# Optimization experiments

Hardware: AMD Instinct MI355X
Metric: run time of the kernel (lower is better)

## Reference

```python
import jax, jax.numpy as jnp
from jax import lax
import numpy as np

K_F = 3                      # propagation kernel
NUM = K_F * K_F - 1          # 8 non-reference neighbors
IDX_REF = NUM // 2           # 4
PROP_TIME = 18
GAMMA = 0.5                  # affinity_gamma (TGASS)
EPS_AFF = 1e-8


def setup_inputs() -> dict:
    key = jax.random.key(0)
    k1, k2, k3, k4, k5 = jax.random.split(key, 5)
    B, H, W = 4, 352, 1216
    feat_init = jax.random.uniform(k1, (B, 1, H, W), jnp.float32) * 10.0   # initial depth
    guidance = jax.random.normal(k2, (B, NUM, H, W), jnp.float32)
    confidence = jax.random.uniform(k3, (B, 1, H, W), jnp.float32)
    # conv_offset_aff: Conv2d(ch_g=8 -> 3*num=24, k=3, pad=1). Zero-init in the
    # module is a training init; use small random weights for a meaningful test.
    w_oa = jax.random.normal(k4, (3 * NUM, NUM, 3, 3), jnp.float32) * 0.05
    b_oa = jax.random.normal(k5, (3 * NUM,), jnp.float32) * 0.01
    aff_scale = jnp.array([GAMMA * NUM], jnp.float32)  # TGASS learnable scale
    return {"feat_init": feat_init, "guidance": guidance, "confidence": confidence,
            "w_oa": w_oa, "b_oa": b_oa, "aff_scale": aff_scale}


def _offset_affinity(guidance, w_oa, b_oa, aff_scale):
    B, _, H, W = guidance.shape
    oa = lax.conv_general_dilated(guidance, w_oa, (1, 1), "SAME",
                                  dimension_numbers=("NCHW", "OIHW", "NCHW"))
    oa = oa + b_oa[None, :, None, None]
    o1, o2, aff = jnp.split(oa, 3, axis=1)            # each [B, 8, H, W]
    offset = jnp.concatenate([o1, o2], axis=1).reshape(B, NUM, 2, H, W)
    zeros_ref = jnp.zeros((B, 1, 2, H, W), offset.dtype)
    offset = jnp.concatenate([offset[:, :IDX_REF], zeros_ref, offset[:, IDX_REF:]],
                             axis=1).reshape(B, -1, H, W)  # [B, 2*9, H, W]
    # TGASS affinity
    aff = jnp.tanh(aff) / (aff_scale[0] + EPS_AFF)
    aff_abs_sum = jnp.sum(jnp.abs(aff), axis=1, keepdims=True) + 1e-4
    aff_abs_sum = jnp.maximum(aff_abs_sum, 1.0)       # TGASS clamp to >= 1
    aff = aff / aff_abs_sum
    aff_ref = 1.0 - jnp.sum(aff, axis=1, keepdims=True)
    aff = jnp.concatenate([aff[:, :IDX_REF], aff_ref, aff[:, IDX_REF:]], axis=1)
    return offset, aff                                 # [B,18,H,W], [B,9,H,W]


def _bilinear(f, ys, xs):
    # f: [H, W]; ys, xs: [K, H, W] float sample coords. Zero outside bounds (DCNv2).
    H, W = f.shape
    y0 = jnp.floor(ys); x0 = jnp.floor(xs)
    wy1 = ys - y0; wy0 = 1.0 - wy1
    wx1 = xs - x0; wx0 = 1.0 - wx1

    def g(yi, xi):
        valid = (yi >= 0) & (yi <= H - 1) & (xi >= 0) & (xi <= W - 1)
        yc = jnp.clip(yi, 0, H - 1).astype(jnp.int32)
        xc = jnp.clip(xi, 0, W - 1).astype(jnp.int32)
        return jnp.where(valid, f[yc, xc], 0.0)

    return (wy0 * wx0 * g(y0, x0) + wy0 * wx1 * g(y0, x0 + 1)
            + wy1 * wx0 * g(y0 + 1, x0) + wy1 * wx1 * g(y0 + 1, x0 + 1))


def _dcn(feat, offset, aff):
    # Modulated deformable conv with w=ones, b=0, stride=1, pad=1, groups=1.
    # feat [B,1,H,W], offset [B,2*9,H,W] ((dy,dx) pairs), aff [B,9,H,W] modulation.
    B, _, H, W = feat.shape
    KK = K_F * K_F
    off = offset.reshape(B, KK, 2, H, W)
    k = jnp.arange(KK)
    ky = (k // K_F - 1).astype(feat.dtype)            # kernel taps, pad=1
    kx = (k % K_F - 1).astype(feat.dtype)
    yg, xg = jnp.meshgrid(jnp.arange(H, dtype=feat.dtype),
                          jnp.arange(W, dtype=feat.dtype), indexing="ij")
    ys = yg[None, None] + ky[None, :, None, None] + off[:, :, 0]  # [B,9,H,W]
    xs = xg[None, None] + kx[None, :, None, None] + off[:, :, 1]
    sampled = jax.vmap(_bilinear)(feat[:, 0], ys, xs)             # [B,9,H,W]
    return jnp.sum(aff * sampled, axis=1, keepdims=True)          # [B,1,H,W]


def reference(feat_init, guidance, confidence, w_oa, b_oa, aff_scale):
    offset, aff = _offset_affinity(guidance, w_oa, b_oa, aff_scale)

    def step(feat, _):
        feat = _dcn(feat * confidence, offset, aff)
        return feat, None

    feat, _ = lax.scan(step, feat_init, None, length=PROP_TIME)
    return feat
```

## Files before the change

### kernel.cpp

```cpp
#include <hip/hip_runtime.h>

#define BB 4
#define HH 352
#define WW 1216
#define HW (HH * WW)
#define NPIX (BB * HW)
#define TX 4

#define PAD_T 5
#define PAD_L 8
#define HP (HH + 2 * PAD_T)
#define WP (WW + 2 * PAD_L)
#define HWP (HP * WP)

#define TROWS 17
#define TCOLS 76
#define TSIZE (TROWS * TCOLS)


__global__ __launch_bounds__(256) void conv_fused_kernel(
    const float* __restrict__ guid, const float* __restrict__ w,
    const float* __restrict__ bias, const float* __restrict__ scale_p,
    unsigned* __restrict__ tab)
{
    int tid = threadIdx.x;
    int bid = blockIdx.x;
    int xcd = bid & 7;
    int u = bid >> 3;
    int role = u & 1;
    int blk = xcd * 209 + (u >> 1);
    int gg = blk * 256 + tid;
    int row = gg / 304;
    int x0 = (gg % 304) * TX;
    int y = row % HH;
    int b = row / HH;
    const float* gb = guid + (size_t)b * 8 * HW;

    if (role == 0) {
        float acc[16][TX];
#pragma unroll
        for (int o = 0; o < 16; ++o) {
            float bv = bias[o];
#pragma unroll
            for (int tx = 0; tx < TX; ++tx) acc[o][tx] = bv;
        }

#pragma unroll 1
        for (int c = 0; c < 8; ++c) {
            float g[3][6];
#pragma unroll
            for (int r = 0; r < 3; ++r) {
                int yy = y + r - 1;
                bool rv = (yy >= 0) && (yy < HH);
                const float* gr = gb + (size_t)c * HW + (size_t)yy * WW;
                if (rv) {
                    const float4 m = *(const float4*)(gr + x0);
                    g[r][1] = m.x; g[r][2] = m.y; g[r][3] = m.z; g[r][4] = m.w;
                    g[r][0] = (x0 > 0) ? gr[x0 - 1] : 0.f;
                    g[r][5] = (x0 + TX < WW) ? gr[x0 + TX] : 0.f;
                } else {
#pragma unroll
                    for (int i = 0; i < 6; ++i) g[r][i] = 0.f;
                }
            }
#pragma unroll
            for (int r = 0; r < 3; ++r) {
#pragma unroll
                for (int i = 0; i < 3; ++i) {
                    int tap = r * 3 + i;
#pragma unroll
                    for (int o = 0; o < 16; ++o) {
                        float wv = w[o * 72 + c * 9 + tap];
#pragma unroll
                        for (int tx = 0; tx < TX; ++tx)
                            acc[o][tx] = fmaf(wv, g[r][i + tx], acc[o][tx]);
                    }
                }
            }
        }

        int idx0 = row * WW + x0;
#pragma unroll
        for (int tx = 0; tx < TX; ++tx) {
            unsigned cw8[8];
#pragma unroll
            for (int n = 0; n < 8; ++n) {
                int k = (n < 4) ? n : n + 1;
                float ky = (float)(k / 3 - 1), kx = (float)(k % 3 - 1);
                float yr = ky + acc[2 * n][tx];
                float xr = kx + acc[2 * n + 1][tx];
                int yq = (int)lrintf((yr + 4.f) * 8192.f);
                int xq = (int)lrintf((xr + 4.f) * 8192.f);
                yq = min(max(yq, 0), 65535);
                xq = min(max(xq, 0), 65535);
                cw8[n] = (unsigned)yq | ((unsigned)xq << 16);
            }
            unsigned* tp = tab + (size_t)(idx0 + tx) * 12;
            *(uint4*)(tp)     = make_uint4(cw8[0], cw8[1], cw8[2], cw8[3]);
            *(uint4*)(tp + 4) = make_uint4(cw8[4], cw8[5], cw8[6], cw8[7]);
        }
    } else {
        float acc[8][TX];
#pragma unroll
        for (int o = 0; o < 8; ++o) {
            float bv = bias[16 + o];
#pragma unroll
            for (int tx = 0; tx < TX; ++tx) acc[o][tx] = bv;
        }

#pragma unroll 1
        for (int c = 0; c < 8; ++c) {
            float g[3][6];
#pragma unroll
            for (int r = 0; r < 3; ++r) {
                int yy = y + r - 1;
                bool rv = (yy >= 0) && (yy < HH);
                const float* gr = gb + (size_t)c * HW + (size_t)yy * WW;
                if (rv) {
                    const float4 m = *(const float4*)(gr + x0);
                    g[r][1] = m.x; g[r][2] = m.y; g[r][3] = m.z; g[r][4] = m.w;
                    g[r][0] = (x0 > 0) ? gr[x0 - 1] : 0.f;
                    g[r][5] = (x0 + TX < WW) ? gr[x0 + TX] : 0.f;
                } else {
#pragma unroll
                    for (int i = 0; i < 6; ++i) g[r][i] = 0.f;
                }
            }
#pragma unroll
            for (int r = 0; r < 3; ++r) {
#pragma unroll
                for (int i = 0; i < 3; ++i) {
                    int tap = r * 3 + i;
#pragma unroll
                    for (int o = 0; o < 8; ++o) {
                        float wv = w[(16 + o) * 72 + c * 9 + tap];
#pragma unroll
                        for (int tx = 0; tx < TX; ++tx)
                            acc[o][tx] = fmaf(wv, g[r][i + tx], acc[o][tx]);
                    }
                }
            }
        }

        float sc = scale_p[0] + 1e-8f;
        int idx0 = row * WW + x0;
#pragma unroll
        for (int tx = 0; tx < TX; ++tx) {
            float a[8];
            float asum = 1e-4f;
#pragma unroll
            for (int n = 0; n < 8; ++n) {
                a[n] = tanhf(acc[n][tx]) / sc;
                asum += fabsf(a[n]);
            }
            asum = fmaxf(asum, 1.0f);
            unsigned q8[8];
#pragma unroll
            for (int n = 0; n < 8; ++n) {
                a[n] = a[n] / asum;
                int q = (int)lrintf((a[n] + 1.f) * 20000.f);
                q = min(max(q, 0), 65535);
                q8[n] = (unsigned)q;
            }
            unsigned* tp = tab + (size_t)(idx0 + tx) * 12 + 8;
            *(uint4*)(tp) = make_uint4(q8[0] | (q8[1] << 16), q8[2] | (q8[3] << 16),
                                       q8[4] | (q8[5] << 16), q8[6] | (q8[7] << 16));
        }
    }
}

template <bool MULCONF>
__global__ __launch_bounds__(512) void prop_step_kernel(
    const float* __restrict__ fsrc, const unsigned* __restrict__ tab,
    const float* __restrict__ conf, float* __restrict__ dst)
{
    __shared__ float tile[TSIZE];

    int bid = blockIdx.x;
    int xcd = bid & 7;
    int s = bid >> 3;
    int gid = xcd * 418 + s;
    int b = gid / 836;
    int r2 = gid % 836;
    int yband = r2 / 19;
    int xb = r2 % 19;
    int t = threadIdx.x;
    int lx = t & 63, ly = t >> 6;
    int x = xb * 64 + lx;
    int y = yband * 8 + ly;
    int idx = (b * HH + y) * WW + x;

    const unsigned* tp = tab + (size_t)idx * 12;
    uint4 t0 = *(const uint4*)(tp);
    uint4 t1 = *(const uint4*)(tp + 4);
    uint4 t2 = *(const uint4*)(tp + 8);
    float cv = MULCONF ? conf[idx] : 0.f;

    {
        const float* gsrc = fsrc + (size_t)b * HWP
                          + (size_t)(yband * 8 + 1) * WP + (xb * 64 + 4);
        for (int i = t; i < TSIZE; i += 512)
            tile[i] = gsrc[(i / TCOLS) * WP + (i % TCOLS)];
    }

    unsigned cw[8] = {t0.x, t0.y, t0.z, t0.w, t1.x, t1.y, t1.z, t1.w};
    float ak[9];
    ak[0] = fmaf((float)(t2.x & 0xffffu), 5e-5f, -1.f);
    ak[1] = fmaf((float)(t2.x >> 16),     5e-5f, -1.f);
    ak[2] = fmaf((float)(t2.y & 0xffffu), 5e-5f, -1.f);
    ak[3] = fmaf((float)(t2.y >> 16),     5e-5f, -1.f);
    ak[5] = fmaf((float)(t2.z & 0xffffu), 5e-5f, -1.f);
    ak[6] = fmaf((float)(t2.z >> 16),     5e-5f, -1.f);
    ak[7] = fmaf((float)(t2.w & 0xffffu), 5e-5f, -1.f);
    ak[8] = fmaf((float)(t2.w >> 16),     5e-5f, -1.f);
    ak[4] = 1.f - (((ak[0] + ak[1]) + (ak[2] + ak[3]))
                 + ((ak[5] + ak[6]) + (ak[7] + ak[8])));

    __syncthreads();

    float fy = (float)ly;
    float fx = (float)lx;
    float res = ak[4] * tile[(ly + 4) * TCOLS + (lx + 4)];
#pragma unroll
    for (int n = 0; n < 8; ++n) {
        float ys = fmaf((float)(cw[n] & 0xffffu), 1.f / 8192.f, fy);
        float xs = fmaf((float)(cw[n] >> 16),     1.f / 8192.f, fx);
        float y0f = floorf(ys), x0f = floorf(xs);
        float wy1 = ys - y0f, wx1 = xs - x0f;
        float wy0 = 1.f - wy1, wx0 = 1.f - wx1;
        int o = (int)y0f * TCOLS + (int)x0f;
        float v00 = tile[o],         v01 = tile[o + 1];
        float v10 = tile[o + TCOLS], v11 = tile[o + TCOLS + 1];
        float sv = wy0 * (wx0 * v00 + wx1 * v01) + wy1 * (wx0 * v10 + wx1 * v11);
        int k = (n < 4) ? n : n + 1;
        res = fmaf(ak[k], sv, res);
    }
    if (MULCONF) {
        res *= cv;
        dst[(size_t)b * HWP + (y + PAD_T) * WP + (x + PAD_L)] = res;
    } else {
        dst[idx] = res;
    }
}

__global__ __launch_bounds__(256) void zero_kernel(float4* __restrict__ p, int n4)
{
    int i = blockIdx.x * blockDim.x + threadIdx.x;
    if (i < n4) p[i] = make_float4(0.f, 0.f, 0.f, 0.f);
}

__global__ __launch_bounds__(256) void mulpad_kernel(
    const float* __restrict__ a, const float* __restrict__ c, float* __restrict__ o)
{
    int t = threadIdx.x;
    int x = blockIdx.x * 64 + (t & 63);
    int y = blockIdx.y * 4 + (t >> 6);
    int b = blockIdx.z;
    int idx = (b * HH + y) * WW + x;
    o[(size_t)b * HWP + (y + PAD_T) * WP + (x + PAD_L)] = a[idx] * c[idx];
}

extern "C" void kernel_launch(void* const* d_in, const int* in_sizes, int n_in,
                              void* d_out, int out_size, void* d_ws, size_t ws_size,
                              hipStream_t stream)
{
    const float* feat_init  = (const float*)d_in[0];
    const float* guidance   = (const float*)d_in[1];
    const float* confidence = (const float*)d_in[2];
    const float* w_oa       = (const float*)d_in[3];
    const float* b_oa       = (const float*)d_in[4];
    const float* aff_scale  = (const float*)d_in[5];
    float* out = (float*)d_out;

    const size_t N = (size_t)NPIX;
    unsigned* tab = (unsigned*)d_ws;
    float* fc0 = (float*)(tab + 12 * N);
    float* fc1 = fc0 + (size_t)BB * HWP;

    const dim3 mgrid(WW / 64, HH / 4, BB);
    const int n4 = 2 * BB * HWP / 4;
    zero_kernel<<<(n4 + 255) / 256, 256, 0, stream>>>((float4*)fc0, n4);
    mulpad_kernel<<<mgrid, 256, 0, stream>>>(feat_init, confidence, fc0);
    conv_fused_kernel<<<2 * 1672, 256, 0, stream>>>(
        guidance, w_oa, b_oa, aff_scale, tab);

    const int pblocks = (WW / 64) * (HH / 8) * BB;
    float* bufs[2] = {fc0, fc1};
    const int T = 18;
    for (int i = 0; i < T; ++i) {
        const float* src = bufs[i & 1];
        if (i < T - 1) {
            float* dst = bufs[(i + 1) & 1];
            prop_step_kernel<true><<<pblocks, 512, 0, stream>>>(
                src, tab, confidence, dst);
        } else {
            prop_step_kernel<false><<<pblocks, 512, 0, stream>>>(
                src, tab, confidence, out);
        }
    }
}
```

Before: 533.7 us.

## Process four tiles per block with double-buffered LDS prefetch; fuse init kernels

```diff
diff --git a/kernel.cpp b/kernel.cpp
--- a/kernel.cpp
+++ b/kernel.cpp
@@ -16,6 +16,7 @@
 #define TROWS 17
 #define TCOLS 76
 #define TSIZE (TROWS * TCOLS)
+#define NTILES 3344
 
 
 __global__ __launch_bounds__(256) void conv_fused_kernel(
@@ -169,58 +170,68 @@
     }
 }
 
+struct TileLoad {
+    uint4 c0, c1, c2;
+    float cf;
+    float r0, r1, r2;
+    int idx;
+    long long poff;
+};
+
 template <bool MULCONF>
-__global__ __launch_bounds__(512) void prop_step_kernel(
+__device__ __forceinline__ TileLoad tile_issue(
+    int gid, int lx, int ly, int t,
     const float* __restrict__ fsrc, const unsigned* __restrict__ tab,
-    const float* __restrict__ conf, float* __restrict__ dst)
-{
-    __shared__ float tile[TSIZE];
-
-    int bid = blockIdx.x;
-    int xcd = bid & 7;
-    int s = bid >> 3;
-    int gid = xcd * 418 + s;
-    int b = gid / 836;
-    int r2 = gid % 836;
-    int yband = r2 / 19;
-    int xb = r2 % 19;
-    int t = threadIdx.x;
-    int lx = t & 63, ly = t >> 6;
-    int x = xb * 64 + lx;
-    int y = yband * 8 + ly;
-    int idx = (b * HH + y) * WW + x;
-
-    const unsigned* tp = tab + (size_t)idx * 12;
-    uint4 t0 = *(const uint4*)(tp);
-    uint4 t1 = *(const uint4*)(tp + 4);
-    uint4 t2 = *(const uint4*)(tp + 8);
-    float cv = MULCONF ? conf[idx] : 0.f;
-
-    {
-        const float* gsrc = fsrc + (size_t)b * HWP
-                          + (size_t)(yband * 8 + 1) * WP + (xb * 64 + 4);
-        for (int i = t; i < TSIZE; i += 512)
-            tile[i] = gsrc[(i / TCOLS) * WP + (i % TCOLS)];
-    }
-
-    unsigned cw[8] = {t0.x, t0.y, t0.z, t0.w, t1.x, t1.y, t1.z, t1.w};
+    const float* __restrict__ conf)
+{
+    TileLoad T;
+    int b = gid / 836, r2 = gid % 836;
+    int yb = r2 / 19, xb = r2 % 19;
+    int x = xb * 64 + lx, y = yb * 8 + ly;
+    T.idx = (b * HH + y) * WW + x;
+    T.poff = (long long)b * HWP + (long long)(y + PAD_T) * WP + (x + PAD_L);
+    const unsigned* tp = tab + (size_t)T.idx * 12;
+    T.c0 = *(const uint4*)(tp);
+    T.c1 = *(const uint4*)(tp + 4);
+    T.c2 = *(const uint4*)(tp + 8);
+    T.cf = MULCONF ? conf[T.idx] : 0.f;
+    const float* gs = fsrc + (size_t)b * HWP
+                    + (size_t)(yb * 8 + 1) * WP + (xb * 64 + 4);
+    T.r0 = gs[(t / TCOLS) * WP + (t % TCOLS)];
+    T.r1 = gs[((t + 512) / TCOLS) * WP + ((t + 512) % TCOLS)];
+    T.r2 = (t + 1024 < TSIZE)
+         ? gs[((t + 1024) / TCOLS) * WP + ((t + 1024) % TCOLS)] : 0.f;
+    return T;
+}
+
+__device__ __forceinline__ void tile_write(float* __restrict__ buf,
+                                           const TileLoad& T, int t)
+{
+    buf[t] = T.r0;
+    buf[t + 512] = T.r1;
+    if (t + 1024 < TSIZE) buf[t + 1024] = T.r2;
+}
+
+template <bool MULCONF>
+__device__ __forceinline__ void tile_compute(
+    const float* __restrict__ buf, const TileLoad& T,
+    float fy, float fx, int ly, int lx, float* __restrict__ dst)
+{
+    unsigned cw[8] = {T.c0.x, T.c0.y, T.c0.z, T.c0.w,
+                      T.c1.x, T.c1.y, T.c1.z, T.c1.w};
     float ak[9];
-    ak[0] = fmaf((float)(t2.x & 0xffffu), 5e-5f, -1.f);
-    ak[1] = fmaf((float)(t2.x >> 16),     5e-5f, -1.f);
-    ak[2] = fmaf((float)(t2.y & 0xffffu), 5e-5f, -1.f);
-    ak[3] = fmaf((float)(t2.y >> 16),     5e-5f, -1.f);
-    ak[5] = fmaf((float)(t2.z & 0xffffu), 5e-5f, -1.f);
-    ak[6] = fmaf((float)(t2.z >> 16),     5e-5f, -1.f);
-    ak[7] = fmaf((float)(t2.w & 0xffffu), 5e-5f, -1.f);
-    ak[8] = fmaf((float)(t2.w >> 16),     5e-5f, -1.f);
+    ak[0] = fmaf((float)(T.c2.x & 0xffffu), 5e-5f, -1.f);
+    ak[1] = fmaf((float)(T.c2.x >> 16),     5e-5f, -1.f);
+    ak[2] = fmaf((float)(T.c2.y & 0xffffu), 5e-5f, -1.f);
+    ak[3] = fmaf((float)(T.c2.y >> 16),     5e-5f, -1.f);
+    ak[5] = fmaf((float)(T.c2.z & 0xffffu), 5e-5f, -1.f);
+    ak[6] = fmaf((float)(T.c2.z >> 16),     5e-5f, -1.f);
+    ak[7] = fmaf((float)(T.c2.w & 0xffffu), 5e-5f, -1.f);
+    ak[8] = fmaf((float)(T.c2.w >> 16),     5e-5f, -1.f);
     ak[4] = 1.f - (((ak[0] + ak[1]) + (ak[2] + ak[3]))
                  + ((ak[5] + ak[6]) + (ak[7] + ak[8])));
 
-    __syncthreads();
-
-    float fy = (float)ly;
-    float fx = (float)lx;
-    float res = ak[4] * tile[(ly + 4) * TCOLS + (lx + 4)];
+    float res = ak[4] * buf[(ly + 4) * TCOLS + (lx + 4)];
 #pragma unroll
     for (int n = 0; n < 8; ++n) {
         float ys = fmaf((float)(cw[n] & 0xffffu), 1.f / 8192.f, fy);
@@ -229,35 +240,93 @@
         float wy1 = ys - y0f, wx1 = xs - x0f;
         float wy0 = 1.f - wy1, wx0 = 1.f - wx1;
         int o = (int)y0f * TCOLS + (int)x0f;
-        float v00 = tile[o],         v01 = tile[o + 1];
-        float v10 = tile[o + TCOLS], v11 = tile[o + TCOLS + 1];
-        float sv = wy0 * (wx0 * v00 + wx1 * v01) + wy1 * (wx0 * v10 + wx1 * v11);
+        float v00 = buf[o],         v01 = buf[o + 1];
+        float v10 = buf[o + TCOLS], v11 = buf[o + TCOLS + 1];
+        float sv = wy0 * (wx0 * v00 + wx1 * v01)
+                 + wy1 * (wx0 * v10 + wx1 * v11);
         int k = (n < 4) ? n : n + 1;
         res = fmaf(ak[k], sv, res);
     }
-    if (MULCONF) {
-        res *= cv;
-        dst[(size_t)b * HWP + (y + PAD_T) * WP + (x + PAD_L)] = res;
-    } else {
-        dst[idx] = res;
-    }
-}
-
-__global__ __launch_bounds__(256) void zero_kernel(float4* __restrict__ p, int n4)
-{
-    int i = blockIdx.x * blockDim.x + threadIdx.x;
-    if (i < n4) p[i] = make_float4(0.f, 0.f, 0.f, 0.f);
-}
-
-__global__ __launch_bounds__(256) void mulpad_kernel(
-    const float* __restrict__ a, const float* __restrict__ c, float* __restrict__ o)
-{
+    if (MULCONF)
+        dst[T.poff] = res * T.cf;
+    else
+        dst[T.idx] = res;
+}
+
+#define LDSBAR() do { \
+    asm volatile("s_waitcnt lgkmcnt(0)" ::: "memory"); \
+    __builtin_amdgcn_s_barrier(); \
+    __builtin_amdgcn_sched_barrier(0); \
+} while (0)
+
+template <bool MULCONF>
+__global__ __launch_bounds__(512) void prop_step_kernel(
+    const float* __restrict__ fsrc, const unsigned* __restrict__ tab,
+    const float* __restrict__ conf, float* __restrict__ dst)
+{
+    __shared__ float buf0[TSIZE];
+    __shared__ float buf1[TSIZE];
+
+    int bid = blockIdx.x;
+    int xcd = bid & 7;
+    int s = bid >> 3;
+    int base = xcd * 418 + 4 * s;
+    bool hasC = (4 * s + 2) < 418;
+    bool hasD = (4 * s + 3) < 418;
     int t = threadIdx.x;
-    int x = blockIdx.x * 64 + (t & 63);
-    int y = blockIdx.y * 4 + (t >> 6);
-    int b = blockIdx.z;
-    int idx = (b * HH + y) * WW + x;
-    o[(size_t)b * HWP + (y + PAD_T) * WP + (x + PAD_L)] = a[idx] * c[idx];
+    int lx = t & 63, ly = t >> 6;
+    float fy = (float)ly, fx = (float)lx;
+
+    TileLoad A = tile_issue<MULCONF>(base,     lx, ly, t, fsrc, tab, conf);
+    TileLoad B = tile_issue<MULCONF>(base + 1, lx, ly, t, fsrc, tab, conf);
+
+    tile_write(buf0, A, t);
+    LDSBAR();
+
+    TileLoad C{};
+    if (hasC) C = tile_issue<MULCONF>(base + 2, lx, ly, t, fsrc, tab, conf);
+    tile_compute<MULCONF>(buf0, A, fy, fx, ly, lx, dst);
+    tile_write(buf1, B, t);
+    LDSBAR();
+
+    TileLoad D{};
+    if (hasD) D = tile_issue<MULCONF>(base + 3, lx, ly, t, fsrc, tab, conf);
+    tile_compute<MULCONF>(buf1, B, fy, fx, ly, lx, dst);
+    if (hasC) tile_write(buf0, C, t);
+    LDSBAR();
+
+    if (hasC) tile_compute<MULCONF>(buf0, C, fy, fx, ly, lx, dst);
+    if (hasD) tile_write(buf1, D, t);
+    LDSBAR();
+
+    if (hasD) tile_compute<MULCONF>(buf1, D, fy, fx, ly, lx, dst);
+}
+
+__global__ __launch_bounds__(256) void init_kernel(
+    const float* __restrict__ feat, const float* __restrict__ conf,
+    float4* __restrict__ fc0, float4* __restrict__ fc1)
+{
+    int i = blockIdx.x * 256 + threadIdx.x;
+    const int q = BB * HWP / 4;
+    if (i >= 2 * q) return;
+    if (i >= q) {
+        fc1[i - q] = make_float4(0.f, 0.f, 0.f, 0.f);
+        return;
+    }
+    int b = i / (HWP / 4);
+    int p4 = i % (HWP / 4);
+    int row = p4 / (WP / 4);
+    int c4 = p4 % (WP / 4);
+    float4 v = make_float4(0.f, 0.f, 0.f, 0.f);
+    if (row >= PAD_T && row < PAD_T + HH && c4 >= 2 && c4 <= 305) {
+        int y = row - PAD_T;
+        int x0 = 4 * c4 - PAD_L;
+        int idx = (b * HH + y) * WW + x0;
+        const float4 f = *(const float4*)(feat + idx);
+        const float4 c = *(const float4*)(conf + idx);
+        v = make_float4(f.x * c.x, f.y * c.y, f.z * c.z, f.w * c.w);
+    }
+    fc0[i] = v;
 }
 
 extern "C" void kernel_launch(void* const* d_in, const int* in_sizes, int n_in,
@@ -277,14 +346,13 @@
     float* fc0 = (float*)(tab + 12 * N);
     float* fc1 = fc0 + (size_t)BB * HWP;
 
-    const dim3 mgrid(WW / 64, HH / 4, BB);
     const int n4 = 2 * BB * HWP / 4;
-    zero_kernel<<<(n4 + 255) / 256, 256, 0, stream>>>((float4*)fc0, n4);
-    mulpad_kernel<<<mgrid, 256, 0, stream>>>(feat_init, confidence, fc0);
+    init_kernel<<<(n4 + 255) / 256, 256, 0, stream>>>(
+        feat_init, confidence, (float4*)fc0, (float4*)fc1);
     conv_fused_kernel<<<2 * 1672, 256, 0, stream>>>(
         guidance, w_oa, b_oa, aff_scale, tab);
 
-    const int pblocks = (WW / 64) * (HH / 8) * BB;
+    const int pblocks = 840;
     float* bufs[2] = {fc0, fc1};
     const int T = 18;
     for (int i = 0; i < T; ++i) {
```

New measurement: 572.7 us. 1.07x slower.
